# Kernel optimization log

Measured on AMD Instinct MI355X. Metric: run time of the kernel, lower is better.

Reference implementation:

```python
import jax, jax.numpy as jnp
import numpy as np

NEG_INF = -1e9  # finite stand-in for Constants.NEG_INF to keep softmax NaN-free


def setup_inputs() -> dict:
    key = jax.random.key(0)
    ks = jax.random.split(key, 6)
    B, Lq, Lk, D = 32, 1024, 1024, 1024
    query = jax.random.normal(ks[0], (B, Lq, D), dtype=jnp.float32)
    context = jax.random.normal(ks[1], (B, Lk, D), dtype=jnp.float32)
    ql = jax.random.randint(ks[2], (B,), 1, Lq + 1).astype(jnp.int32)
    cl = jax.random.randint(ks[3], (B,), 1, Lk + 1).astype(jnp.int32)
    # pad_packed_sequence pads to the max length in batch -> force max present
    ql = ql.at[0].set(Lq)
    cl = cl.at[0].set(Lk)
    W_in = jax.random.normal(ks[4], (D, D), dtype=jnp.float32) * (D ** -0.5)
    W_out = jax.random.normal(ks[5], (D, 2 * D), dtype=jnp.float32) * ((2 * D) ** -0.5)
    return {"query": query, "context": context, "query_lengths": ql,
            "context_lengths": cl, "W_in": W_in, "W_out": W_out}


def reference(query, context, query_lengths, context_lengths, W_in, W_out):
    B, Lq, D = query.shape
    Lk = context.shape[1]
    # attention_type == 'general': project queries
    q = jnp.einsum('bqd,ed->bqe', query, W_in)                      # [B,Lq,D]
    scores = jnp.einsum('bqd,bkd->bqk', q, context)                 # [B,Lq,Lk]
    # pack/pad round-trips == length mask on both query and context axes
    qmask = jnp.arange(Lq)[None, :] < query_lengths[:, None]        # [B,Lq]
    kmask = jnp.arange(Lk)[None, :] < context_lengths[:, None]      # [B,Lk]
    mask = qmask[:, :, None] & kmask[:, None, :]                    # [B,Lq,Lk]
    scores_m = jnp.where(mask, scores, NEG_INF)
    weights = jax.nn.softmax(scores_m, axis=2)
    mix = jnp.einsum('bqk,bkd->bqd', weights, context)              # [B,Lq,D]
    combined = jnp.concatenate([mix, q], axis=2)                    # [B,Lq,2D]
    output = jnp.tanh(jnp.einsum('bqc,dc->bqd', combined, W_out))   # [B,Lq,D]
    return output, scores_m
```

## Files before the change

kernel.cpp:

```cpp
#include <hip/hip_runtime.h>
#include <math.h>

#define BM 128
#define BN 128
#define BK 32
#define KP 40

typedef __bf16 bf16x8 __attribute__((ext_vector_type(8)));
typedef float  floatx4 __attribute__((ext_vector_type(4)));
typedef unsigned short u16;

__device__ __forceinline__ u16 f2bf(float x) {
    unsigned int u = __float_as_uint(x);
    u += 0x7FFFu + ((u >> 16) & 1u);
    return (u16)(u >> 16);
}
__device__ __forceinline__ float bf2f(u16 h) {
    return __uint_as_float(((unsigned int)h) << 16);
}

__device__ __forceinline__ void bar_lds() {
    asm volatile("s_waitcnt lgkmcnt(0)" ::: "memory");
    __builtin_amdgcn_s_barrier();
}

template <bool LO>
__device__ __forceinline__ void cvt_store(u16* H, u16* L, int idx, float4 v) {
    u16 h0 = f2bf(v.x), h1 = f2bf(v.y), h2 = f2bf(v.z), h3 = f2bf(v.w);
    *(ushort4*)(H + idx) = make_ushort4(h0, h1, h2, h3);
    if (LO) {
        u16 l0 = f2bf(v.x - bf2f(h0)), l1 = f2bf(v.y - bf2f(h1));
        u16 l2 = f2bf(v.z - bf2f(h2)), l3 = f2bf(v.w - bf2f(h3));
        *(ushort4*)(L + idx) = make_ushort4(l0, l1, l2, l3);
    }
}

enum OpMode { OP_F32 = 0, OP_PLANES = 1, OP_BF16 = 2 };

template <int EPI, bool SOFTA, bool SPLITA, bool TRANSB, int NPASS, int AMODE, int BMODE>
__global__ __launch_bounds__(256, 2) void mfma_gemm(
    const void* __restrict__ Av, const void* __restrict__ A2v,
    const void* __restrict__ Bv, const void* __restrict__ B2v,
    void* __restrict__ Cv, void* __restrict__ C2v,
    int K, int lda, int ldb, int ldc,
    long long aBatch, long long bBatch, long long cBatch,
    const float2* __restrict__ stats, long long statsBatch,
    const int* __restrict__ qlen, const int* __restrict__ klen)
{
    const int b = blockIdx.z;

    const float* A_f  = (const float*)Av + aBatch * b;
    const u16*   A_h  = (const u16*)Av + aBatch * b;
    const u16*   A_l  = (const u16*)A2v + aBatch * b;
    const u16*   A2_h = (const u16*)A2v;
    const float* B_f  = (const float*)Bv + bBatch * b;
    const u16*   B_h  = (const u16*)Bv + bBatch * b;
    const u16*   B_l  = (const u16*)B2v + bBatch * b;

    constexpr int LP = (NPASS == 3) ? 2 : 1;
    __shared__ __align__(16) u16 smem[(BM + BN) * KP * LP];
    u16* Ah = smem;
    u16* Al = Ah + (NPASS == 3 ? BM * KP : 0);
    u16* Bh = Ah + BM * KP * LP;
    u16* Bl = Bh + (NPASS == 3 ? BN * KP : 0);

    const int tid = threadIdx.x;
    const int m0 = blockIdx.y * BM;
    const int n0 = blockIdx.x * BN;

    const int sr = tid >> 3;
    const int sc = (tid & 7) << 2;

    const int wv = tid >> 6;
    const int wm = (wv >> 1) << 6;
    const int wn = (wv & 1) << 6;
    const int lane = tid & 63;
    const int lm = lane & 15;
    const int lk = (lane >> 4) << 3;

    floatx4 acc[4][4];
#pragma unroll
    for (int i = 0; i < 4; i++)
#pragma unroll
        for (int j = 0; j < 4; j++) acc[i][j] = (floatx4)0.f;

    float2 st[4];
    if (SOFTA) {
        const float2* sp = stats + statsBatch * b;
#pragma unroll
        for (int r = 0; r < 4; r++) st[r] = sp[m0 + (r << 5) + sr];
    }

    struct PF {
        float4  vaf[4]; ushort4 vah[4], vaL[4];
        float4  vbf[4]; ushort4 vbh[4], vbL[4];
    };

    auto ldA = [&](int k0, PF& r_) {
        if constexpr (AMODE == OP_F32) {
#pragma unroll
            for (int r = 0; r < 4; r++) {
                const int row = (r << 5) + sr;
                r_.vaf[r] = *(const float4*)(A_f + (size_t)(m0 + row) * lda + k0 + sc);
            }
        } else if constexpr (AMODE == OP_PLANES) {
#pragma unroll
            for (int r = 0; r < 4; r++) {
                const int row = (r << 5) + sr;
                const size_t off = (size_t)(m0 + row) * lda + k0 + sc;
                r_.vah[r] = *(const ushort4*)(A_h + off);
                r_.vaL[r] = *(const ushort4*)(A_l + off);
            }
        } else {
            const u16* Ap = A_h;
            int kk = k0;
            if constexpr (SPLITA) {
                const int half = K >> 1;
                Ap = (k0 < half) ? A_h : A2_h;
                kk = k0 & (half - 1);
            }
#pragma unroll
            for (int r = 0; r < 4; r++) {
                const int row = (r << 5) + sr;
                r_.vah[r] = *(const ushort4*)(Ap + (size_t)(m0 + row) * lda + kk + sc);
            }
        }
    };
    auto ldB = [&](int k0, PF& r_) {
        if constexpr (TRANSB) {
            const int kr = tid >> 3;
            const int c4 = (tid & 7) << 2;
#pragma unroll
            for (int r = 0; r < 4; r++) {
                const int col = (r << 5) + c4;
                const float* src = B_f + (size_t)(k0 + kr) * ldb + n0 + col;
                float2 v0 = *(const float2*)(src);
                float2 v1 = *(const float2*)(src + 2);
                r_.vbf[r] = make_float4(v0.x, v0.y, v1.x, v1.y);
            }
        } else if constexpr (BMODE == OP_F32) {
#pragma unroll
            for (int r = 0; r < 4; r++) {
                const int row = (r << 5) + sr;
                r_.vbf[r] = *(const float4*)(B_f + (size_t)(n0 + row) * ldb + k0 + sc);
            }
        } else if constexpr (BMODE == OP_PLANES) {
#pragma unroll
            for (int r = 0; r < 4; r++) {
                const int row = (r << 5) + sr;
                const size_t off = (size_t)(n0 + row) * ldb + k0 + sc;
                r_.vbh[r] = *(const ushort4*)(B_h + off);
                r_.vbL[r] = *(const ushort4*)(B_l + off);
            }
        } else {
#pragma unroll
            for (int r = 0; r < 4; r++) {
                const int row = (r << 5) + sr;
                r_.vbh[r] = *(const ushort4*)(B_h + (size_t)(n0 + row) * ldb + k0 + sc);
            }
        }
    };
    auto stA = [&](const PF& r_) {
#pragma unroll
        for (int r = 0; r < 4; r++) {
            const int idx = ((r << 5) + sr) * KP + sc;
            if constexpr (AMODE == OP_F32) {
                float4 v = r_.vaf[r];
                if (SOFTA) {
                    v.x = expf(v.x - st[r].x) * st[r].y;
                    v.y = expf(v.y - st[r].x) * st[r].y;
                    v.z = expf(v.z - st[r].x) * st[r].y;
                    v.w = expf(v.w - st[r].x) * st[r].y;
                }
                cvt_store<NPASS == 3>(Ah, Al, idx, v);
            } else if constexpr (AMODE == OP_PLANES) {
                *(ushort4*)(Ah + idx) = r_.vah[r];
                *(ushort4*)(Al + idx) = r_.vaL[r];
            } else {
                *(ushort4*)(Ah + idx) = r_.vah[r];
            }
        }
    };
    auto stB = [&](const PF& r_) {
        if constexpr (TRANSB) {
            const int kr = tid >> 3;
            const int c4 = (tid & 7) << 2;
#pragma unroll
            for (int r = 0; r < 4; r++) {
                const int col = (r << 5) + c4;
                const float4 v = r_.vbf[r];
                Bh[(col + 0) * KP + kr] = f2bf(v.x);
                Bh[(col + 1) * KP + kr] = f2bf(v.y);
                Bh[(col + 2) * KP + kr] = f2bf(v.z);
                Bh[(col + 3) * KP + kr] = f2bf(v.w);
            }
        } else {
#pragma unroll
            for (int r = 0; r < 4; r++) {
                const int idx = ((r << 5) + sr) * KP + sc;
                if constexpr (BMODE == OP_F32) {
                    cvt_store<NPASS == 3>(Bh, Bl, idx, r_.vbf[r]);
                } else if constexpr (BMODE == OP_PLANES) {
                    *(ushort4*)(Bh + idx) = r_.vbh[r];
                    *(ushort4*)(Bl + idx) = r_.vbL[r];
                } else {
                    *(ushort4*)(Bh + idx) = r_.vbh[r];
                }
            }
        }
    };
    auto frags_mfma = [&]() {
        bf16x8 ah[4], al[4], bh[4], bl[4];
#pragma unroll
        for (int t = 0; t < 4; t++) {
            const int ar = (wm + (t << 4) + lm) * KP + lk;
            ah[t] = *(const bf16x8*)(Ah + ar);
            if constexpr (NPASS == 3) al[t] = *(const bf16x8*)(Al + ar);
        }
#pragma unroll
        for (int t = 0; t < 4; t++) {
            const int br = (wn + (t << 4) + lm) * KP + lk;
            bh[t] = *(const bf16x8*)(Bh + br);
            if constexpr (NPASS == 3) bl[t] = *(const bf16x8*)(Bl + br);
        }
#pragma unroll
        for (int i = 0; i < 4; i++)
#pragma unroll
            for (int j = 0; j < 4; j++) {
                if constexpr (NPASS == 3) {
                    acc[i][j] = __builtin_amdgcn_mfma_f32_16x16x32_bf16(al[i], bh[j], acc[i][j], 0, 0, 0);
                    acc[i][j] = __builtin_amdgcn_mfma_f32_16x16x32_bf16(ah[i], bl[j], acc[i][j], 0, 0, 0);
                }
                acc[i][j] = __builtin_amdgcn_mfma_f32_16x16x32_bf16(ah[i], bh[j], acc[i][j], 0, 0, 0);
            }
    };

    PF r0, r1;
    ldA(0, r0);  ldB(0, r0);
    ldA(BK, r1); ldB(BK, r1);

    for (int k0 = 0; k0 < K; k0 += 2 * BK) {
        stA(r0); stB(r0);
        bar_lds();
        if (k0 + 2 * BK < K) { ldA(k0 + 2 * BK, r0); ldB(k0 + 2 * BK, r0); }
        frags_mfma();
        bar_lds();
        stA(r1); stB(r1);
        bar_lds();
        if (k0 + 3 * BK < K) { ldA(k0 + 3 * BK, r1); ldB(k0 + 3 * BK, r1); }
        frags_mfma();
        bar_lds();
    }

    float* C_f = (float*)Cv + cBatch * b;
    u16*   C_h = (u16*)Cv + cBatch * b;
    u16*   C_l = (u16*)C2v + cBatch * b;
    int qb = 0, kb = 0;
    if (EPI == 1) { qb = qlen[b]; kb = klen[b]; }
    const int qd = (lane >> 4) << 2;
#pragma unroll
    for (int i = 0; i < 4; i++)
#pragma unroll
        for (int j = 0; j < 4; j++) {
            const int col = n0 + wn + (j << 4) + lm;
#pragma unroll
            for (int r = 0; r < 4; r++) {
                const int row = m0 + wm + (i << 4) + qd + r;
                const size_t off = (size_t)row * ldc + col;
                float v = acc[i][j][r];
                if constexpr (EPI == 0) {
                    C_f[off] = v;
                } else if constexpr (EPI == 1) {
                    C_f[off] = (row < qb && col < kb) ? v : -1e9f;
                } else if constexpr (EPI == 2) {
                    C_f[off] = tanhf(v);
                } else if constexpr (EPI == 3) {
                    const u16 h = f2bf(v);
                    C_h[off] = h;
                    C_l[off] = f2bf(v - bf2f(h));
                } else {
                    C_h[off] = f2bf(v);
                }
            }
        }
}

__global__ __launch_bounds__(256) void row_stats_kernel(
    const float* __restrict__ S, float2* __restrict__ stats, int L)
{
    const int row = blockIdx.x * 4 + (threadIdx.x >> 6);
    const int lane = threadIdx.x & 63;
    const float* p = S + (size_t)row * L;

    float mx = -1e30f;
    for (int j = lane; j < L; j += 64) mx = fmaxf(mx, p[j]);
#pragma unroll
    for (int off = 32; off > 0; off >>= 1) mx = fmaxf(mx, __shfl_xor(mx, off, 64));

    float sm = 0.f;
    for (int j = lane; j < L; j += 64) sm += expf(p[j] - mx);
#pragma unroll
    for (int off = 32; off > 0; off >>= 1) sm += __shfl_xor(sm, off, 64);

    if (lane == 0) stats[row] = make_float2(mx, 1.f / sm);
}

__global__ __launch_bounds__(256) void cvt_hilo_kernel(
    const float* __restrict__ s, u16* __restrict__ hi, u16* __restrict__ lo, int n4)
{
    const int stride = gridDim.x * 256;
    for (int i = blockIdx.x * 256 + threadIdx.x; i < n4; i += stride) {
        float4 v = ((const float4*)s)[i];
        u16 h0 = f2bf(v.x), h1 = f2bf(v.y), h2 = f2bf(v.z), h3 = f2bf(v.w);
        ((ushort4*)hi)[i] = make_ushort4(h0, h1, h2, h3);
        ((ushort4*)lo)[i] = make_ushort4(f2bf(v.x - bf2f(h0)), f2bf(v.y - bf2f(h1)),
                                         f2bf(v.z - bf2f(h2)), f2bf(v.w - bf2f(h3)));
    }
}
__global__ __launch_bounds__(256) void cvt_bf16_kernel(
    const float* __restrict__ s, u16* __restrict__ d, int n4)
{
    const int stride = gridDim.x * 256;
    for (int i = blockIdx.x * 256 + threadIdx.x; i < n4; i += stride) {
        float4 v = ((const float4*)s)[i];
        ((ushort4*)d)[i] = make_ushort4(f2bf(v.x), f2bf(v.y), f2bf(v.z), f2bf(v.w));
    }
}

extern "C" void kernel_launch(void* const* d_in, const int* in_sizes, int n_in,
                              void* d_out, int out_size, void* d_ws, size_t ws_size,
                              hipStream_t stream)
{
    const float* query   = (const float*)d_in[0];
    const float* context = (const float*)d_in[1];
    const int*   qlens   = (const int*)d_in[2];
    const int*   clens   = (const int*)d_in[3];
    const float* W_in    = (const float*)d_in[4];
    const float* W_out   = (const float*)d_in[5];

    const int B = 32, Lq = 1024, Lk = 1024, D = 1024;
    const long long nQ = (long long)B * Lq * D;

    float* out    = (float*)d_out;
    float* scores = out + nQ;

    u16* q_hi    = (u16*)d_ws;
    u16* q_lo    = q_hi + nQ;
    u16* mixb    = q_lo + nQ;
    u16* w_in_hi = mixb + nQ;
    u16* w_in_lo = w_in_hi + (1 << 20);
    u16* w_out_b = w_in_lo + (1 << 20);
    float2* stats = (float2*)(w_out_b + (2 << 20));

    cvt_hilo_kernel<<<1024, 256, 0, stream>>>(W_in, w_in_hi, w_in_lo, (D * D) / 4);
    cvt_bf16_kernel<<<2048, 256, 0, stream>>>(W_out, w_out_b, (D * 2 * D) / 4);

    mfma_gemm<3, false, false, false, 3, OP_F32, OP_PLANES>
        <<<dim3(D / BN, (B * Lq) / BM, 1), 256, 0, stream>>>(
        query, nullptr, w_in_hi, w_in_lo, q_hi, q_lo,
        D, D, D, D, 0LL, 0LL, 0LL, nullptr, 0LL, nullptr, nullptr);

    mfma_gemm<1, false, false, false, 3, OP_PLANES, OP_F32>
        <<<dim3(Lk / BN, Lq / BM, B), 256, 0, stream>>>(
        q_hi, q_lo, context, nullptr, scores, nullptr,
        D, D, D, Lk, (long long)Lq * D, (long long)Lk * D, (long long)Lq * Lk,
        nullptr, 0LL, qlens, clens);

    row_stats_kernel<<<(B * Lq) / 4, 256, 0, stream>>>(scores, stats, Lk);

    mfma_gemm<4, true, false, true, 1, OP_F32, OP_F32>
        <<<dim3(D / BN, Lq / BM, B), 256, 0, stream>>>(
        scores, nullptr, context, nullptr, mixb, nullptr,
        Lk, Lk, D, D, (long long)Lq * Lk, (long long)Lk * D, (long long)Lq * D,
        stats, (long long)Lq, nullptr, nullptr);

    mfma_gemm<2, false, true, false, 1, OP_BF16, OP_BF16>
        <<<dim3(D / BN, (B * Lq) / BM, 1), 256, 0, stream>>>(
        mixb, q_hi, w_out_b, nullptr, out, nullptr,
        2 * D, D, 2 * D, D, 0LL, 0LL, 0LL, nullptr, 0LL, nullptr, nullptr);
}
```

Baseline: 1.401 ms.

## Skip masked tiles in scores GEMM and truncate K loop in mix GEMM

In the scores GEMM, tiles that lie entirely outside the valid query or context length now write the -1e9 fill and return early, skipping the MFMA work. In the softmax-weighted mix GEMM, blocks whose rows are all within the query length stop the K loop at the context length rounded up to 2*BK, since the remaining columns carry zero softmax weight. Padded rows still run the full K loop so their uniform weights are reproduced. Correctness relies on masked scores giving exactly zero weight after exponentiation.

```diff
diff --git a/kernel.cpp b/kernel.cpp
--- a/kernel.cpp
+++ b/kernel.cpp
@@ -49,6 +49,48 @@
 {
     const int b = blockIdx.z;
 
+    const int tid = threadIdx.x;
+    const int m0 = blockIdx.y * BM;
+    const int n0 = blockIdx.x * BN;
+
+    const int wv = tid >> 6;
+    const int wm = (wv >> 1) << 6;
+    const int wn = (wv & 1) << 6;
+    const int lane = tid & 63;
+    const int lm = lane & 15;
+    const int lk = (lane >> 4) << 3;
+    const int qd = (lane >> 4) << 2;
+
+    int qb = 0, kb = 0;
+    if constexpr (EPI == 1) {
+        qb = qlen[b]; kb = klen[b];
+        if (m0 >= qb || n0 >= kb) {
+            float* C_f0 = (float*)Cv + cBatch * b;
+#pragma unroll
+            for (int i = 0; i < 4; i++)
+#pragma unroll
+                for (int j = 0; j < 4; j++) {
+                    const int col = n0 + wn + (j << 4) + lm;
+#pragma unroll
+                    for (int r = 0; r < 4; r++) {
+                        const int row = m0 + wm + (i << 4) + qd + r;
+                        C_f0[(size_t)row * ldc + col] = -1e9f;
+                    }
+                }
+            return;
+        }
+    }
+
+    int Kend = K;
+    if constexpr (SOFTA) {
+        const int ql2 = qlen[b];
+        if (m0 + BM <= ql2) {
+            const int kl2 = klen[b];
+            int ke = ((kl2 + 2 * BK - 1) / (2 * BK)) * (2 * BK);
+            Kend = ke < K ? ke : K;
+        }
+    }
+
     const float* A_f  = (const float*)Av + aBatch * b;
     const u16*   A_h  = (const u16*)Av + aBatch * b;
     const u16*   A_l  = (const u16*)A2v + aBatch * b;
@@ -64,19 +106,8 @@
     u16* Bh = Ah + BM * KP * LP;
     u16* Bl = Bh + (NPASS == 3 ? BN * KP : 0);
 
-    const int tid = threadIdx.x;
-    const int m0 = blockIdx.y * BM;
-    const int n0 = blockIdx.x * BN;
-
     const int sr = tid >> 3;
     const int sc = (tid & 7) << 2;
-
-    const int wv = tid >> 6;
-    const int wm = (wv >> 1) << 6;
-    const int wn = (wv & 1) << 6;
-    const int lane = tid & 63;
-    const int lm = lane & 15;
-    const int lk = (lane >> 4) << 3;
 
     floatx4 acc[4][4];
 #pragma unroll
@@ -239,15 +270,15 @@
     ldA(0, r0);  ldB(0, r0);
     ldA(BK, r1); ldB(BK, r1);
 
-    for (int k0 = 0; k0 < K; k0 += 2 * BK) {
+    for (int k0 = 0; k0 < Kend; k0 += 2 * BK) {
         stA(r0); stB(r0);
         bar_lds();
-        if (k0 + 2 * BK < K) { ldA(k0 + 2 * BK, r0); ldB(k0 + 2 * BK, r0); }
+        if (k0 + 2 * BK < Kend) { ldA(k0 + 2 * BK, r0); ldB(k0 + 2 * BK, r0); }
         frags_mfma();
         bar_lds();
         stA(r1); stB(r1);
         bar_lds();
-        if (k0 + 3 * BK < K) { ldA(k0 + 3 * BK, r1); ldB(k0 + 3 * BK, r1); }
+        if (k0 + 3 * BK < Kend) { ldA(k0 + 3 * BK, r1); ldB(k0 + 3 * BK, r1); }
         frags_mfma();
         bar_lds();
     }
@@ -255,9 +286,6 @@
     float* C_f = (float*)Cv + cBatch * b;
     u16*   C_h = (u16*)Cv + cBatch * b;
     u16*   C_l = (u16*)C2v + cBatch * b;
-    int qb = 0, kb = 0;
-    if (EPI == 1) { qb = qlen[b]; kb = klen[b]; }
-    const int qd = (lane >> 4) << 2;
 #pragma unroll
     for (int i = 0; i < 4; i++)
 #pragma unroll
@@ -372,7 +400,7 @@
         <<<dim3(D / BN, Lq / BM, B), 256, 0, stream>>>(
         scores, nullptr, context, nullptr, mixb, nullptr,
         Lk, Lk, D, D, (long long)Lq * Lk, (long long)Lk * D, (long long)Lq * D,
-        stats, (long long)Lq, nullptr, nullptr);
+        stats, (long long)Lq, qlens, clens);
 
     mfma_gemm<2, false, true, false, 1, OP_BF16, OP_BF16>
         <<<dim3(D / BN, (B * Lq) / BM, 1), 256, 0, stream>>>(
```

Measured after the change: 1.305 ms. -6.9%, faster.
